# Performance work log

Hardware: AMD Instinct MI355X
Metric: run time of the kernel (lower is better)

Reference implementation:

```python
import jax, jax.numpy as jnp
import numpy as np

NUM_HEADS = 8
EPS = 1e-3

N_TOKENS = 32768
DIM = 256
N_WIN = 128
WIN = N_TOKENS // N_WIN  # 256 tokens per window


def setup_inputs() -> dict:
    key = jax.random.key(0)
    ks = jax.random.split(key, 4)
    x = jax.random.normal(ks[0], (N_TOKENS, DIM), dtype=jnp.float32)
    # torch nn.Linear weights are [out_features, in_features]
    w_qkv = jax.random.normal(ks[1], (3 * DIM, DIM), dtype=jnp.float32) * (DIM ** -0.5)
    w_proj = jax.random.normal(ks[2], (DIM, DIM), dtype=jnp.float32) * (DIM ** -0.5)
    b_proj = jnp.zeros((DIM,), dtype=jnp.float32)
    batch_win_inds = (jnp.arange(N_TOKENS) // WIN).astype(jnp.int64)
    offsets = (jnp.arange(N_WIN) * WIN).astype(jnp.int64)
    counts = jnp.full((N_WIN,), WIN, dtype=jnp.int64)
    return {"x": x, "w_qkv": w_qkv, "w_proj": w_proj, "b_proj": b_proj,
            "offsets": offsets, "counts": counts, "batch_win_inds": batch_win_inds}


def reference(x, w_qkv, w_proj, b_proj, offsets, counts, batch_win_inds):
    N, C = x.shape
    H = NUM_HEADS
    hd = C // H
    W = counts.shape[0]  # number of windows (static)

    qkv = x @ w_qkv.T                      # [N, 3C]
    q, k, v = jnp.split(qkv, 3, axis=-1)   # each [N, C]
    q = jax.nn.relu(q.reshape(N, H, hd))   # [N, H, hd]
    k = jax.nn.relu(k.reshape(N, H, hd))
    v = v.reshape(N, H, hd)

    seg = batch_win_inds.astype(jnp.int32)
    # per-window KV state: kv[w] = sum_{i in w} k_i^T v_i   -> [W, H, hd, hd]
    kv = jax.ops.segment_sum(jnp.einsum('nhc,nhd->nhcd', k, v), seg, num_segments=W)
    # per-window key sum for normalizer                      -> [W, H, hd]
    s = jax.ops.segment_sum(k, seg, num_segments=W)

    y = jnp.einsum('nhc,nhcd->nhd', q, kv[seg])              # [N, H, hd]
    z = jnp.sum(s[seg] * q, axis=-1, keepdims=True)          # [N, H, 1]
    y = y / (z + EPS)

    y = y.reshape(N, C) @ w_proj.T + b_proj                  # [N, C]
    return y
```

## Files before the change

kernel.cpp:

```cpp
#include <hip/hip_runtime.h>

typedef __bf16 bf16_t;
typedef bf16_t bf16x8 __attribute__((ext_vector_type(8)));
typedef bf16_t bf16x4 __attribute__((ext_vector_type(4)));
typedef float f32x4 __attribute__((ext_vector_type(4)));

#define M_TOK 32768
#define NWIN 128
#define WIN  256

typedef __attribute__((address_space(3))) void* as3p;
typedef const __attribute__((address_space(1))) void* as1p;

__device__ __forceinline__ void gll16(const void* g, void* l) {
    __builtin_amdgcn_global_load_lds((as1p)g, (as3p)l, 16, 0, 0);
}

__device__ __forceinline__ bf16x8 cvt8(f32x4 a, f32x4 b) {
    bf16x8 o;
    o[0] = (bf16_t)a[0]; o[1] = (bf16_t)a[1]; o[2] = (bf16_t)a[2]; o[3] = (bf16_t)a[3];
    o[4] = (bf16_t)b[0]; o[5] = (bf16_t)b[1]; o[6] = (bf16_t)b[2]; o[7] = (bf16_t)b[3];
    return o;
}

__global__ __launch_bounds__(256) void convpack(
    const float* __restrict__ X, const float* __restrict__ wq, const float* __restrict__ wp,
    bf16_t* __restrict__ Xb, bf16_t* __restrict__ wqb, bf16_t* __restrict__ wpb)
{
    long i8 = ((long)blockIdx.x * 256 + threadIdx.x) * 8;
    const float* s; bf16_t* dst; long idx;
    if (i8 < 8388608)      { s = X;  dst = Xb;  idx = i8; }
    else if (i8 < 8585216) { s = wq; dst = wqb; idx = i8 - 8388608; }
    else                   { s = wp; dst = wpb; idx = i8 - 8585216; }
    f32x4 v0 = *(const f32x4*)(s + idx);
    f32x4 v1 = *(const f32x4*)(s + idx + 4);
    *(bf16x8*)(dst + idx) = cvt8(v0, v1);
}

__global__ __launch_bounds__(256) void gemm1_qkv(
    const bf16_t* __restrict__ Xb,
    const bf16_t* __restrict__ Wb,
    bf16_t* __restrict__ QKV)
{
    __shared__ __align__(16) bf16_t As[128][64];
    __shared__ __align__(16) bf16_t Bs[128][64];

    const int tid = threadIdx.x;
    const int lane = tid & 63;
    const int wv = tid >> 6;
    const int wm = wv >> 1, wn = wv & 1;
    const int id = blockIdx.x;
    const int sg = id / 48, wsub = id % 48;
    const int m0 = (sg * 8 + (wsub & 7)) * 128;
    const int n0 = (wsub >> 3) * 128;
    const int r = lane & 15, q = lane >> 4;
    const int lrow = lane >> 3;
    const int lg8 = ((lane & 7) ^ lrow) * 8;
    const int rx = r & 7;

    f32x4 acc[4][4] = {};

    for (int kc = 0; kc < 256; kc += 64) {
#pragma unroll
        for (int g = 0; g < 4; ++g) {
            const int rb = wv * 32 + g * 8;
            gll16(Xb + (size_t)(m0 + rb + lrow) * 256 + kc + lg8, &As[rb][0]);
            gll16(Wb + (size_t)(n0 + rb + lrow) * 256 + kc + lg8, &Bs[rb][0]);
        }
        __syncthreads();

#pragma unroll
        for (int kk = 0; kk < 64; kk += 32) {
            const int ax8 = (((kk >> 3) + q) ^ rx) * 8;
            bf16x8 a[4], b[4];
#pragma unroll
            for (int i = 0; i < 4; ++i)
                a[i] = *(const bf16x8*)&As[wm * 64 + i * 16 + r][ax8];
#pragma unroll
            for (int j = 0; j < 4; ++j)
                b[j] = *(const bf16x8*)&Bs[wn * 64 + j * 16 + r][ax8];
#pragma unroll
            for (int i = 0; i < 4; ++i)
#pragma unroll
                for (int j = 0; j < 4; ++j)
                    acc[i][j] = __builtin_amdgcn_mfma_f32_16x16x32_bf16(b[j], a[i], acc[i][j], 0, 0, 0);
        }
        __syncthreads();
    }

#pragma unroll
    for (int i = 0; i < 4; ++i) {
        const int rowg = m0 + wm * 64 + i * 16 + r;
#pragma unroll
        for (int j = 0; j < 4; ++j) {
            const int nb = n0 + wn * 64 + j * 16 + q * 4;
            const int nblk = nb >> 5, d = nb & 31;
            bf16x4 o;
#pragma unroll
            for (int reg = 0; reg < 4; ++reg) {
                float v = acc[i][j][reg];
                if (nblk < 16) v = fmaxf(v, 0.0f);
                o[reg] = (bf16_t)v;
            }
            *(bf16x4*)&QKV[((size_t)nblk * M_TOK + rowg) * 32 + d] = o;
        }
    }
}

__global__ __launch_bounds__(256) void gemm2_proj(
    const bf16_t* __restrict__ Y,
    const bf16_t* __restrict__ Wb,
    const float* __restrict__ bias,
    float* __restrict__ Out)
{
    __shared__ __align__(16) bf16_t As[128][64];
    __shared__ __align__(16) bf16_t Bs[64][64];

    const int tid = threadIdx.x;
    const int lane = tid & 63;
    const int wv = tid >> 6;
    const int wm = wv >> 1, wn = wv & 1;
    const int id = blockIdx.x;
    const int sg = id / 32, wsub = id % 32;
    const int m0 = (sg * 8 + (wsub & 7)) * 128;
    const int n0 = (wsub >> 3) * 64;
    const int r = lane & 15, q = lane >> 4;
    const int lrow = lane >> 3;
    const int lg8 = ((lane & 7) ^ lrow) * 8;
    const int rx = r & 7;

    f32x4 acc[4][2] = {};

    for (int kc = 0; kc < 256; kc += 64) {
#pragma unroll
        for (int g = 0; g < 4; ++g) {
            const int rb = wv * 32 + g * 8;
            gll16(Y + (size_t)(m0 + rb + lrow) * 256 + kc + lg8, &As[rb][0]);
        }
#pragma unroll
        for (int g = 0; g < 2; ++g) {
            const int rb = wv * 16 + g * 8;
            gll16(Wb + (size_t)(n0 + rb + lrow) * 256 + kc + lg8, &Bs[rb][0]);
        }
        __syncthreads();

#pragma unroll
        for (int kk = 0; kk < 64; kk += 32) {
            const int ax8 = (((kk >> 3) + q) ^ rx) * 8;
            bf16x8 a[4], b[2];
#pragma unroll
            for (int i = 0; i < 4; ++i)
                a[i] = *(const bf16x8*)&As[wm * 64 + i * 16 + r][ax8];
#pragma unroll
            for (int j = 0; j < 2; ++j)
                b[j] = *(const bf16x8*)&Bs[wn * 32 + j * 16 + r][ax8];
#pragma unroll
            for (int i = 0; i < 4; ++i)
#pragma unroll
                for (int j = 0; j < 2; ++j)
                    acc[i][j] = __builtin_amdgcn_mfma_f32_16x16x32_bf16(b[j], a[i], acc[i][j], 0, 0, 0);
        }
        __syncthreads();
    }

#pragma unroll
    for (int i = 0; i < 4; ++i) {
        const int rowg = m0 + wm * 64 + i * 16 + r;
#pragma unroll
        for (int j = 0; j < 2; ++j) {
            const int nb = n0 + wn * 32 + j * 16 + q * 4;
            f32x4 bi = *(const f32x4*)(bias + nb);
            f32x4 o;
#pragma unroll
            for (int reg = 0; reg < 4; ++reg) o[reg] = acc[i][j][reg] + bi[reg];
            *(f32x4*)&Out[(size_t)rowg * 256 + nb] = o;
        }
    }
}

__global__ __launch_bounds__(256) void kvy_kernel(
    const bf16_t* __restrict__ QKV,
    const int* __restrict__ offsets,
    const int* __restrict__ counts,
    bf16_t* __restrict__ Y)
{
    const int w = blockIdx.x;
    const int h = blockIdx.y;
    const int is64 = (counts[1] == 0) ? 1 : 0;
    const int off = offsets[w << is64];
    const int tid = threadIdx.x;
    const int lane = tid & 63;
    const int wv = tid >> 6;

    __shared__ __align__(16) bf16_t KT[32 * 264];
    __shared__ __align__(16) bf16_t VT[32 * 264];
    __shared__ __align__(16) bf16_t KVT[32 * 40];
    __shared__ float sbuf[32];
    __shared__ float spart[32 * 8];
    __shared__ float zinv[WIN];

    {
        const int t = tid;
        const bf16_t* kp = QKV + ((size_t)(8 + h) * M_TOK + off + t) * 32;
        const bf16_t* vp = QKV + ((size_t)(16 + h) * M_TOK + off + t) * 32;
        bf16_t ka[32], va[32];
#pragma unroll
        for (int u = 0; u < 4; ++u) {
            bf16x8 kk = *(const bf16x8*)(kp + u * 8);
            bf16x8 vvv = *(const bf16x8*)(vp + u * 8);
#pragma unroll
            for (int j = 0; j < 8; ++j) { ka[u * 8 + j] = kk[j]; va[u * 8 + j] = vvv[j]; }
        }
#pragma unroll
        for (int c = 0; c < 32; ++c) {
            KT[c * 264 + t] = ka[c];
            VT[c * 264 + t] = va[c];
        }
    }
    __syncthreads();

    {
        const int c = tid >> 3;
        const int tc = (tid & 7) * 32;
        float ps = 0.f;
#pragma unroll
        for (int u = 0; u < 4; ++u) {
            bf16x8 kk = *(const bf16x8*)(&KT[c * 264 + tc + u * 8]);
#pragma unroll
            for (int j = 0; j < 8; ++j) ps += (float)kk[j];
        }
        spart[c * 8 + (tid & 7)] = ps;
    }
    {
        const int i = wv >> 1, j = wv & 1;
        const int r = lane & 15, q = lane >> 4;
        f32x4 acc = {};
#pragma unroll
        for (int ch = 0; ch < 8; ++ch) {
            bf16x8 af = *(const bf16x8*)(&KT[(i * 16 + r) * 264 + ch * 32 + q * 8]);
            bf16x8 bf_ = *(const bf16x8*)(&VT[(j * 16 + r) * 264 + ch * 32 + q * 8]);
            acc = __builtin_amdgcn_mfma_f32_16x16x32_bf16(af, bf_, acc, 0, 0, 0);
        }
        bf16x4 kv4;
#pragma unroll
        for (int reg = 0; reg < 4; ++reg) kv4[reg] = (bf16_t)acc[reg];
        *(bf16x4*)(&KVT[(j * 16 + r) * 40 + i * 16 + q * 4]) = kv4;
    }
    __syncthreads();
    if (tid < 32) {
        float s = 0.f;
#pragma unroll
        for (int u = 0; u < 8; ++u) s += spart[tid * 8 + u];
        sbuf[tid] = s;
    }
    __syncthreads();

    {
        const int t = tid;
        const bf16_t* qp = QKV + ((size_t)h * M_TOK + off + t) * 32;
        float z = 0.f;
#pragma unroll
        for (int u = 0; u < 4; ++u) {
            bf16x8 qq = *(const bf16x8*)(qp + u * 8);
#pragma unroll
            for (int j = 0; j < 8; ++j) z += (float)qq[j] * sbuf[u * 8 + j];
        }
        zinv[t] = 1.0f / (z + 1e-3f);
    }
    __syncthreads();

    {
        const int r = lane & 15, q = lane >> 4;
        bf16x8 b0 = *(const bf16x8*)(&KVT[(r) * 40 + q * 8]);
        bf16x8 b1 = *(const bf16x8*)(&KVT[(16 + r) * 40 + q * 8]);
#pragma unroll
        for (int u = 0; u < 4; ++u) {
            const int mi = wv * 4 + u;
            const bf16_t* ap = QKV + ((size_t)h * M_TOK + off + mi * 16 + r) * 32 + q * 8;
            bf16x8 af = *(const bf16x8*)ap;
            f32x4 acc0 = {}, acc1 = {};
            acc0 = __builtin_amdgcn_mfma_f32_16x16x32_bf16(b0, af, acc0, 0, 0, 0);
            acc1 = __builtin_amdgcn_mfma_f32_16x16x32_bf16(b1, af, acc1, 0, 0, 0);
            const int tkn = mi * 16 + r;
            const float zi = zinv[tkn];
            bf16_t* yp = Y + (size_t)(off + tkn) * 256 + h * 32;
            bf16x4 o0, o1;
#pragma unroll
            for (int reg = 0; reg < 4; ++reg) {
                o0[reg] = (bf16_t)(acc0[reg] * zi);
                o1[reg] = (bf16_t)(acc1[reg] * zi);
            }
            *(bf16x4*)(yp + q * 4) = o0;
            *(bf16x4*)(yp + 16 + q * 4) = o1;
        }
    }
}

extern "C" void kernel_launch(void* const* d_in, const int* in_sizes, int n_in,
                              void* d_out, int out_size, void* d_ws, size_t ws_size,
                              hipStream_t stream) {
    const float* x      = (const float*)d_in[0];
    const float* w_qkv  = (const float*)d_in[1];
    const float* w_proj = (const float*)d_in[2];
    const float* b_proj = (const float*)d_in[3];
    const int*   offs   = (const int*)d_in[4];
    const int*   cnts   = (const int*)d_in[5];

    char* ws = (char*)d_ws;
    bf16_t* QKV = (bf16_t*)ws;
    bf16_t* Y   = (bf16_t*)(ws + 50331648);
    bf16_t* Xb  = Y;
    bf16_t* Wqb = (bf16_t*)(ws + 67108864);
    bf16_t* Wpb = (bf16_t*)(ws + 67502080);
    float*  out = (float*)d_out;

    convpack<<<4224, 256, 0, stream>>>(x, w_qkv, w_proj, Xb, Wqb, Wpb);

    gemm1_qkv<<<1536, 256, 0, stream>>>(Xb, Wqb, QKV);

    kvy_kernel<<<dim3(NWIN, 8), 256, 0, stream>>>(QKV, offs, cnts, Y);

    gemm2_proj<<<1024, 256, 0, stream>>>(Y, Wpb, b_proj, out);
}
```

Before: 138.6 us.

## Fuse X fp32-to-bf16 conversion into QKV GEMM and double-buffer both GEMMs

```diff
diff --git a/kernel.cpp b/kernel.cpp
--- a/kernel.cpp
+++ b/kernel.cpp
@@ -23,27 +23,27 @@
     return o;
 }
 
-__global__ __launch_bounds__(256) void convpack(
-    const float* __restrict__ X, const float* __restrict__ wq, const float* __restrict__ wp,
-    bf16_t* __restrict__ Xb, bf16_t* __restrict__ wqb, bf16_t* __restrict__ wpb)
+__global__ __launch_bounds__(256) void wconv(
+    const float* __restrict__ wq, const float* __restrict__ wp,
+    bf16_t* __restrict__ wqb, bf16_t* __restrict__ wpb)
 {
-    long i8 = ((long)blockIdx.x * 256 + threadIdx.x) * 8;
-    const float* s; bf16_t* dst; long idx;
-    if (i8 < 8388608)      { s = X;  dst = Xb;  idx = i8; }
-    else if (i8 < 8585216) { s = wq; dst = wqb; idx = i8 - 8388608; }
-    else                   { s = wp; dst = wpb; idx = i8 - 8585216; }
-    f32x4 v0 = *(const f32x4*)(s + idx);
-    f32x4 v1 = *(const f32x4*)(s + idx + 4);
-    *(bf16x8*)(dst + idx) = cvt8(v0, v1);
+    int i4 = (blockIdx.x * 256 + threadIdx.x) * 4;
+    const float* s; bf16_t* dst; int idx;
+    if (i4 < 196608) { s = wq; dst = wqb; idx = i4; }
+    else             { s = wp; dst = wpb; idx = i4 - 196608; }
+    f32x4 v = *(const f32x4*)(s + idx);
+    bf16x4 o;
+    o[0] = (bf16_t)v[0]; o[1] = (bf16_t)v[1]; o[2] = (bf16_t)v[2]; o[3] = (bf16_t)v[3];
+    *(bf16x4*)(dst + idx) = o;
 }
 
 __global__ __launch_bounds__(256) void gemm1_qkv(
-    const bf16_t* __restrict__ Xb,
+    const float* __restrict__ X,
     const bf16_t* __restrict__ Wb,
     bf16_t* __restrict__ QKV)
 {
-    __shared__ __align__(16) bf16_t As[128][64];
-    __shared__ __align__(16) bf16_t Bs[128][64];
+    __shared__ __align__(16) bf16_t As[2][128][32];
+    __shared__ __align__(16) bf16_t Bs[2][128][32];
 
     const int tid = threadIdx.x;
     const int lane = tid & 63;
@@ -54,39 +54,66 @@
     const int m0 = (sg * 8 + (wsub & 7)) * 128;
     const int n0 = (wsub >> 3) * 128;
     const int r = lane & 15, q = lane >> 4;
-    const int lrow = lane >> 3;
-    const int lg8 = ((lane & 7) ^ lrow) * 8;
-    const int rx = r & 7;
+    const int lrow = lane >> 2;
+    const int lcol = lane & 3;
+    const int sgr = (lcol ^ ((lane >> 3) & 3)) * 8;
+    const int ax8 = (q ^ ((r >> 1) & 3)) * 8;
 
     f32x4 acc[4][4] = {};
 
-    for (int kc = 0; kc < 256; kc += 64) {
-#pragma unroll
-        for (int g = 0; g < 4; ++g) {
-            const int rb = wv * 32 + g * 8;
-            gll16(Xb + (size_t)(m0 + rb + lrow) * 256 + kc + lg8, &As[rb][0]);
-            gll16(Wb + (size_t)(n0 + rb + lrow) * 256 + kc + lg8, &Bs[rb][0]);
-        }
+    auto loadA = [&](int kc, f32x4 (&ar)[2][2]) {
+#pragma unroll
+        for (int g = 0; g < 2; ++g) {
+            const float* src = X + (size_t)(m0 + wv * 32 + g * 16 + lrow) * 256 + kc + sgr;
+            ar[g][0] = *(const f32x4*)src;
+            ar[g][1] = *(const f32x4*)(src + 4);
+        }
+    };
+    auto stageB = [&](int kc, int buf) {
+#pragma unroll
+        for (int g = 0; g < 2; ++g)
+            gll16(Wb + (size_t)(n0 + wv * 32 + g * 16 + lrow) * 256 + kc + sgr,
+                  &Bs[buf][wv * 32 + g * 16][0]);
+    };
+    auto writeA = [&](f32x4 (&ar)[2][2], int buf) {
+#pragma unroll
+        for (int g = 0; g < 2; ++g)
+            *(bf16x8*)&As[buf][wv * 32 + g * 16 + lrow][lcol * 8] = cvt8(ar[g][0], ar[g][1]);
+    };
+    auto compute = [&](int buf) {
+        bf16x8 a[4], b[4];
+#pragma unroll
+        for (int i = 0; i < 4; ++i)
+            a[i] = *(const bf16x8*)&As[buf][wm * 64 + i * 16 + r][ax8];
+#pragma unroll
+        for (int j = 0; j < 4; ++j)
+            b[j] = *(const bf16x8*)&Bs[buf][wn * 64 + j * 16 + r][ax8];
+#pragma unroll
+        for (int i = 0; i < 4; ++i)
+#pragma unroll
+            for (int j = 0; j < 4; ++j)
+                acc[i][j] = __builtin_amdgcn_mfma_f32_16x16x32_bf16(b[j], a[i], acc[i][j], 0, 0, 0);
+    };
+
+    {
+        f32x4 ar[2][2];
+        loadA(0, ar);
+        stageB(0, 0);
+        writeA(ar, 0);
+    }
+    __syncthreads();
+
+#pragma unroll
+    for (int t = 0; t < 7; ++t) {
+        const int cur = t & 1, nxt = cur ^ 1;
+        f32x4 ar[2][2];
+        loadA((t + 1) * 32, ar);
+        stageB((t + 1) * 32, nxt);
+        compute(cur);
+        writeA(ar, nxt);
         __syncthreads();
-
-#pragma unroll
-        for (int kk = 0; kk < 64; kk += 32) {
-            const int ax8 = (((kk >> 3) + q) ^ rx) * 8;
-            bf16x8 a[4], b[4];
-#pragma unroll
-            for (int i = 0; i < 4; ++i)
-                a[i] = *(const bf16x8*)&As[wm * 64 + i * 16 + r][ax8];
-#pragma unroll
-            for (int j = 0; j < 4; ++j)
-                b[j] = *(const bf16x8*)&Bs[wn * 64 + j * 16 + r][ax8];
-#pragma unroll
-            for (int i = 0; i < 4; ++i)
-#pragma unroll
-                for (int j = 0; j < 4; ++j)
-                    acc[i][j] = __builtin_amdgcn_mfma_f32_16x16x32_bf16(b[j], a[i], acc[i][j], 0, 0, 0);
-        }
-        __syncthreads();
-    }
+    }
+    compute(1);
 
 #pragma unroll
     for (int i = 0; i < 4; ++i) {
@@ -113,8 +140,8 @@
     const float* __restrict__ bias,
     float* __restrict__ Out)
 {
-    __shared__ __align__(16) bf16_t As[128][64];
-    __shared__ __align__(16) bf16_t Bs[64][64];
+    __shared__ __align__(16) bf16_t As[2][128][32];
+    __shared__ __align__(16) bf16_t Bs[2][64][32];
 
     const int tid = threadIdx.x;
     const int lane = tid & 63;
@@ -125,43 +152,45 @@
     const int m0 = (sg * 8 + (wsub & 7)) * 128;
     const int n0 = (wsub >> 3) * 64;
     const int r = lane & 15, q = lane >> 4;
-    const int lrow = lane >> 3;
-    const int lg8 = ((lane & 7) ^ lrow) * 8;
-    const int rx = r & 7;
+    const int lrow = lane >> 2;
+    const int sgr = ((lane & 3) ^ ((lane >> 3) & 3)) * 8;
+    const int ax8 = (q ^ ((r >> 1) & 3)) * 8;
 
     f32x4 acc[4][2] = {};
 
-    for (int kc = 0; kc < 256; kc += 64) {
-#pragma unroll
-        for (int g = 0; g < 4; ++g) {
-            const int rb = wv * 32 + g * 8;
-            gll16(Y + (size_t)(m0 + rb + lrow) * 256 + kc + lg8, &As[rb][0]);
-        }
-#pragma unroll
-        for (int g = 0; g < 2; ++g) {
-            const int rb = wv * 16 + g * 8;
-            gll16(Wb + (size_t)(n0 + rb + lrow) * 256 + kc + lg8, &Bs[rb][0]);
-        }
+    auto stage = [&](int kc, int buf) {
+#pragma unroll
+        for (int g = 0; g < 2; ++g)
+            gll16(Y + (size_t)(m0 + wv * 32 + g * 16 + lrow) * 256 + kc + sgr,
+                  &As[buf][wv * 32 + g * 16][0]);
+        gll16(Wb + (size_t)(n0 + wv * 16 + lrow) * 256 + kc + sgr,
+              &Bs[buf][wv * 16][0]);
+    };
+    auto compute = [&](int buf) {
+        bf16x8 a[4], b[2];
+#pragma unroll
+        for (int i = 0; i < 4; ++i)
+            a[i] = *(const bf16x8*)&As[buf][wm * 64 + i * 16 + r][ax8];
+#pragma unroll
+        for (int j = 0; j < 2; ++j)
+            b[j] = *(const bf16x8*)&Bs[buf][wn * 32 + j * 16 + r][ax8];
+#pragma unroll
+        for (int i = 0; i < 4; ++i)
+#pragma unroll
+            for (int j = 0; j < 2; ++j)
+                acc[i][j] = __builtin_amdgcn_mfma_f32_16x16x32_bf16(b[j], a[i], acc[i][j], 0, 0, 0);
+    };
+
+    stage(0, 0);
+    __syncthreads();
+#pragma unroll
+    for (int t = 0; t < 7; ++t) {
+        const int cur = t & 1, nxt = cur ^ 1;
+        stage((t + 1) * 32, nxt);
+        compute(cur);
         __syncthreads();
-
-#pragma unroll
-        for (int kk = 0; kk < 64; kk += 32) {
-            const int ax8 = (((kk >> 3) + q) ^ rx) * 8;
-            bf16x8 a[4], b[2];
-#pragma unroll
-            for (int i = 0; i < 4; ++i)
-                a[i] = *(const bf16x8*)&As[wm * 64 + i * 16 + r][ax8];
-#pragma unroll
-            for (int j = 0; j < 2; ++j)
-                b[j] = *(const bf16x8*)&Bs[wn * 32 + j * 16 + r][ax8];
-#pragma unroll
-            for (int i = 0; i < 4; ++i)
-#pragma unroll
-                for (int j = 0; j < 2; ++j)
-                    acc[i][j] = __builtin_amdgcn_mfma_f32_16x16x32_bf16(b[j], a[i], acc[i][j], 0, 0, 0);
-        }
-        __syncthreads();
-    }
+    }
+    compute(1);
 
 #pragma unroll
     for (int i = 0; i < 4; ++i) {
@@ -309,14 +338,13 @@
     char* ws = (char*)d_ws;
     bf16_t* QKV = (bf16_t*)ws;
     bf16_t* Y   = (bf16_t*)(ws + 50331648);
-    bf16_t* Xb  = Y;
     bf16_t* Wqb = (bf16_t*)(ws + 67108864);
     bf16_t* Wpb = (bf16_t*)(ws + 67502080);
     float*  out = (float*)d_out;
 
-    convpack<<<4224, 256, 0, stream>>>(x, w_qkv, w_proj, Xb, Wqb, Wpb);
-
-    gemm1_qkv<<<1536, 256, 0, stream>>>(Xb, Wqb, QKV);
+    wconv<<<256, 256, 0, stream>>>(w_qkv, w_proj, Wqb, Wpb);
+
+    gemm1_qkv<<<1536, 256, 0, stream>>>(x, Wqb, QKV);
 
     kvy_kernel<<<dim3(NWIN, 8), 256, 0, stream>>>(QKV, offs, cnts, Y);
 
```

Measured after the change: 149.2 us. +7.6%, slower.
